# Kernel optimization log

Measured on AMD Instinct MI355X. Metric: run time of the kernel, lower is better.

## Reference

```python
import jax, jax.numpy as jnp
import numpy as np

B = 16384          # batch
S = 510            # no_of_states
D = 2 * S + 4      # 1024, context width
HID = 512          # self.hidden_size
H = 1024           # no_of_heads
INHIB = 3.0        # kWTA inhibition coefficient


def _lin(x, W, b):
    # torch nn.Linear convention: W is [out, in]
    return x @ W.T + b


def kwta(x, kw):
    """Per-row dynamic-k winner-take-all.
    k_i = argmax(kw[i]); top-k entries of x[i] kept, the rest divided by INHIB.
    Vectorized replacement for the original per-row topk + scatter loop."""
    k = jnp.argmax(kw, axis=1)                         # [B] per-row k
    s = -jnp.sort(-x, axis=1)                          # descending sort per row
    idx = jnp.clip(k - 1, 0, x.shape[1] - 1)
    thr = jnp.take_along_axis(s, idx[:, None], axis=1)  # k-th largest value
    mask = (x >= thr) & (k[:, None] > 0)               # winners (k=0 -> none)
    return jnp.where(mask, x, x / INHIB)


def setup_inputs() -> dict:
    key = jax.random.key(0)
    ks = jax.random.split(key, 30)

    def n(k, shape, s=0.02):
        return (jax.random.normal(k, shape) * s).astype(jnp.float32)

    return {
        "input": jax.random.normal(ks[0], (B, S), jnp.float32),
        "task_indicator": jax.random.normal(ks[1], (B, S + 4), jnp.float32),
        "hidden": jax.random.normal(ks[2], (1, B, D), jnp.float32),
        # Elman RNN step (single layer, hidden width D)
        "w_ih": n(ks[3], (D, D)), "b_ih": n(ks[4], (D,)),
        "w_hh": n(ks[5], (D, D)), "b_hh": n(ks[6], (D,)),
        # context gating heads
        "w_cx11": n(ks[7], (2 * HID, D)), "b_cx11": n(ks[8], (2 * HID,)),
        "w_cx12": n(ks[9], (2 * HID, 2 * HID)), "b_cx12": n(ks[10], (2 * HID,)),
        "w_cx21": n(ks[11], (HID, D)), "b_cx21": n(ks[12], (HID,)),
        "w_cx22": n(ks[13], (HID, HID)), "b_cx22": n(ks[14], (HID,)),
        "w_cx31": n(ks[15], (H, D)), "b_cx31": n(ks[16], (H,)),
        "w_cx32": n(ks[17], (H, H)), "b_cx32": n(ks[18], (H,)),
        # main MLP stack
        "w_l1": n(ks[19], (2 * HID, D)), "b_l1": n(ks[20], (2 * HID,)),
        "w_l2": n(ks[21], (HID, 2 * HID)), "b_l2": n(ks[22], (HID,)),
        "w_l3": n(ks[23], (H, HID)), "b_l3": n(ks[24], (H,)),
        "w_l4": n(ks[25], (H, H)), "b_l4": n(ks[26], (H,)),
    }


def reference(input, task_indicator, hidden,
              w_ih, b_ih, w_hh, b_hh,
              w_cx11, b_cx11, w_cx12, b_cx12,
              w_cx21, b_cx21, w_cx22, b_cx22,
              w_cx31, b_cx31, w_cx32, b_cx32,
              w_l1, b_l1, w_l2, b_l2, w_l3, b_l3, w_l4, b_l4):
    ctx = jnp.concatenate([input, task_indicator], axis=1)      # [B, D]
    h0 = hidden[0]                                              # [B, D]
    # Elman RNN step: out == next hidden state
    out = jnp.tanh(ctx @ w_ih.T + b_ih + h0 @ w_hh.T + b_hh)    # [B, D]
    next_hidden = out[:, None, :]                               # transpose(0,1) of [1,B,D]

    cx1 = jax.nn.softmax(_lin(jnp.tanh(_lin(out, w_cx11, b_cx11)), w_cx12, b_cx12), axis=1)
    cx2 = jax.nn.softmax(_lin(jnp.tanh(_lin(out, w_cx21, b_cx21)), w_cx22, b_cx22), axis=1)
    cx3 = jax.nn.softmax(_lin(jnp.tanh(_lin(out, w_cx31, b_cx31)), w_cx32, b_cx32), axis=1)

    x = _lin(out, w_l1, b_l1)        # [B, 2*HID]
    x = kwta(x, cx1)
    x = _lin(x, w_l2, b_l2)          # [B, HID]
    x = kwta(x, cx2)
    x = _lin(x, w_l3, b_l3)          # [B, H]
    x = kwta(x, cx3)
    x = _lin(x, w_l4, b_l4)          # [B, H]
    return (x, next_hidden)
```

## Files before the change

kernel.cpp:

```cpp
#include <hip/hip_runtime.h>
#include <math.h>

#define BB 16384
#define BM 128
#define BN 128
#define BK 32

__global__ __launch_bounds__(256) void concat_kernel(const float* __restrict__ inp,
    const float* __restrict__ task, float* __restrict__ ctx)
{
  int idx = blockIdx.x * 256 + threadIdx.x;
  int b = idx >> 10;
  int c = idx & 1023;
  float v;
  if (c < 510) v = inp[(size_t)b * 510 + c];
  else         v = task[(size_t)b * 514 + (c - 510)];
  ctx[idx] = v;
}

template<bool TANH, bool CIN>
__global__ __launch_bounds__(256) void gemm32g_kernel(
    const float* __restrict__ A, const float* __restrict__ W,
    const float* __restrict__ b1, const float* __restrict__ b2,
    const float* __restrict__ Cin, float* __restrict__ C,
    int N, int K, int lda, int ldw, unsigned foldmask)
{
  __shared__ float As[BK * BM];
  __shared__ float Bs[BK * BN];
  const int tid = threadIdx.x;
  const int tx = tid & 15;
  const int ty = tid >> 4;
  const int m0 = blockIdx.x * BM;
  const int n0 = blockIdx.y * BN;
  const int rrow = tid >> 3;
  const int kc = (tid & 7) << 2;

  float res[2][2][4][4], cur[2][2][4][4];
#pragma unroll
  for (int g = 0; g < 2; ++g)
#pragma unroll
    for (int h = 0; h < 2; ++h)
#pragma unroll
      for (int i = 0; i < 4; ++i)
#pragma unroll
        for (int j = 0; j < 4; ++j) { res[g][h][i][j] = 0.f; cur[g][h][i][j] = 0.f; }

  float4 ra[4], rb[4];
  const int NT = K / BK;

#pragma unroll
  for (int i = 0; i < 4; ++i) {
    int r = rrow + (i << 5);
    ra[i] = *(const float4*)(A + (size_t)(m0 + r) * lda + kc);
    rb[i] = *(const float4*)(W + (size_t)(n0 + r) * ldw + kc);
  }

  for (int kt = 0; kt < NT; ++kt) {
    __syncthreads();
#pragma unroll
    for (int i = 0; i < 4; ++i) {
      int cS = (rrow + (i << 5)) ^ kc;
      As[(kc + 0) * BM + cS] = ra[i].x;
      As[(kc + 1) * BM + cS] = ra[i].y;
      As[(kc + 2) * BM + cS] = ra[i].z;
      As[(kc + 3) * BM + cS] = ra[i].w;
      Bs[(kc + 0) * BN + cS] = rb[i].x;
      Bs[(kc + 1) * BN + cS] = rb[i].y;
      Bs[(kc + 2) * BN + cS] = rb[i].z;
      Bs[(kc + 3) * BN + cS] = rb[i].w;
    }
    __syncthreads();
    if (kt + 1 < NT) {
      int kb = (kt + 1) * BK;
#pragma unroll
      for (int i = 0; i < 4; ++i) {
        int r = rrow + (i << 5);
        ra[i] = *(const float4*)(A + (size_t)(m0 + r) * lda + kb + kc);
        rb[i] = *(const float4*)(W + (size_t)(n0 + r) * ldw + kb + kc);
      }
    }
#pragma unroll 8
    for (int kk = 0; kk < BK; ++kk) {
      const int swz = kk & 28;
      const float4 a0 = *(const float4*)&As[kk * BM + ((4 * ty) ^ swz)];
      const float4 a1 = *(const float4*)&As[kk * BM + 64 + ((4 * ty) ^ swz)];
      const float4 b0 = *(const float4*)&Bs[kk * BN + ((4 * tx) ^ swz)];
      const float4 b1r = *(const float4*)&Bs[kk * BN + 64 + ((4 * tx) ^ swz)];
      const float av[2][4] = {{a0.x, a0.y, a0.z, a0.w}, {a1.x, a1.y, a1.z, a1.w}};
      const float wv[2][4] = {{b0.x, b0.y, b0.z, b0.w}, {b1r.x, b1r.y, b1r.z, b1r.w}};
#pragma unroll
      for (int g = 0; g < 2; ++g)
#pragma unroll
        for (int h = 0; h < 2; ++h)
#pragma unroll
          for (int i = 0; i < 4; ++i)
#pragma unroll
            for (int j = 0; j < 4; ++j)
              cur[g][h][i][j] = fmaf(av[g][i], wv[h][j], cur[g][h][i][j]);
    }
    if ((foldmask >> kt) & 1u) {
#pragma unroll
      for (int g = 0; g < 2; ++g)
#pragma unroll
        for (int h = 0; h < 2; ++h)
#pragma unroll
          for (int i = 0; i < 4; ++i)
#pragma unroll
            for (int j = 0; j < 4; ++j) {
              res[g][h][i][j] = res[g][h][i][j] + cur[g][h][i][j];
              cur[g][h][i][j] = 0.f;
            }
    }
  }

  float4 b1v[2], b2v[2];
#pragma unroll
  for (int h = 0; h < 2; ++h) {
    int cb = n0 + h * 64 + 4 * tx;
    b1v[h] = b1 ? *(const float4*)&b1[cb] : make_float4(0.f, 0.f, 0.f, 0.f);
    b2v[h] = (CIN && b2) ? *(const float4*)&b2[cb] : make_float4(0.f, 0.f, 0.f, 0.f);
  }
#pragma unroll
  for (int g = 0; g < 2; ++g)
#pragma unroll
    for (int i = 0; i < 4; ++i) {
      int row = m0 + g * 64 + 4 * ty + i;
#pragma unroll
      for (int h = 0; h < 2; ++h) {
        int col = n0 + h * 64 + 4 * tx;
        float4 o;
        if (CIN) {
          float4 ci = *(const float4*)&Cin[(size_t)row * N + col];
          o.x = ((ci.x + b1v[h].x) + res[g][h][i][0]) + b2v[h].x;
          o.y = ((ci.y + b1v[h].y) + res[g][h][i][1]) + b2v[h].y;
          o.z = ((ci.z + b1v[h].z) + res[g][h][i][2]) + b2v[h].z;
          o.w = ((ci.w + b1v[h].w) + res[g][h][i][3]) + b2v[h].w;
        } else if (b1) {
          o.x = res[g][h][i][0] + b1v[h].x;
          o.y = res[g][h][i][1] + b1v[h].y;
          o.z = res[g][h][i][2] + b1v[h].z;
          o.w = res[g][h][i][3] + b1v[h].w;
        } else {
          o.x = res[g][h][i][0]; o.y = res[g][h][i][1];
          o.z = res[g][h][i][2]; o.w = res[g][h][i][3];
        }
        if (TANH) {
          o.x = (float)tanh((double)o.x);
          o.y = (float)tanh((double)o.y);
          o.z = (float)tanh((double)o.z);
          o.w = (float)tanh((double)o.w);
        }
        *(float4*)&C[(size_t)row * N + col] = o;
      }
    }
}

template<int NELEM>
__global__ __launch_bounds__(256) void kwta_kernel(const float* __restrict__ x,
    const float* __restrict__ cxz, float* __restrict__ out)
{
  constexpr int NPER = NELEM / 256;
  const int row = blockIdx.x;
  const int tid = threadIdx.x;
  const float* xr = x + (size_t)row * NELEM;
  const float* zr = cxz + (size_t)row * NELEM;
  float* orow = out + (size_t)row * NELEM;

  __shared__ float es[NELEM];
  __shared__ float red[256];
  __shared__ int   ri[256];
  __shared__ float bs[8];
  __shared__ float ssum;
  __shared__ unsigned hist[256];
  __shared__ unsigned cum[256];
  __shared__ int selBin;
  __shared__ unsigned selBase;

  float zv[NPER];
  float mx = -INFINITY;
#pragma unroll
  for (int j = 0; j < NPER; ++j) {
    zv[j] = zr[tid + (j << 8)];
    mx = fmaxf(mx, zv[j]);
  }
  red[tid] = mx;
  __syncthreads();
  for (int s = 128; s > 0; s >>= 1) {
    if (tid < s) red[tid] = fmaxf(red[tid], red[tid + s]);
    __syncthreads();
  }
  mx = red[0];
  __syncthreads();

  float ev[NPER];
#pragma unroll
  for (int j = 0; j < NPER; ++j) {
    float d = zv[j] - mx;
    ev[j] = (float)exp((double)d);
    es[tid + (j << 8)] = ev[j];
  }
  __syncthreads();

  if (tid < NELEM / 128) {
    const float* a = &es[tid * 128];
    float r0 = a[0], r1 = a[1], r2 = a[2], r3 = a[3];
    float r4 = a[4], r5 = a[5], r6 = a[6], r7 = a[7];
    for (int i = 8; i < 128; i += 8) {
      r0 += a[i + 0]; r1 += a[i + 1]; r2 += a[i + 2]; r3 += a[i + 3];
      r4 += a[i + 4]; r5 += a[i + 5]; r6 += a[i + 6]; r7 += a[i + 7];
    }
    bs[tid] = ((r0 + r1) + (r2 + r3)) + ((r4 + r5) + (r6 + r7));
  }
  __syncthreads();
  if (tid == 0) {
    float s;
    if (NELEM == 1024)
      s = ((bs[0] + bs[1]) + (bs[2] + bs[3])) + ((bs[4] + bs[5]) + (bs[6] + bs[7]));
    else
      s = (bs[0] + bs[1]) + (bs[2] + bs[3]);
    ssum = s;
  }
  __syncthreads();
  const float s = ssum;

  float bv = -INFINITY; int bi = 0x7fffffff;
#pragma unroll
  for (int j = 0; j < NPER; ++j) {
    float u = ev[j] / s;
    int i = tid + (j << 8);
    if (u > bv) { bv = u; bi = i; }
  }
  red[tid] = bv; ri[tid] = bi;
  __syncthreads();
  for (int st = 128; st > 0; st >>= 1) {
    if (tid < st) {
      float ov = red[tid + st]; int oi = ri[tid + st];
      if (ov > red[tid] || (ov == red[tid] && oi < ri[tid])) { red[tid] = ov; ri[tid] = oi; }
    }
    __syncthreads();
  }
  const int k = ri[0];

  float xv[NPER]; unsigned key[NPER];
#pragma unroll
  for (int j = 0; j < NPER; ++j) {
    float v = xr[tid + (j << 8)];
    xv[j] = v;
    unsigned sb = __float_as_uint(v);
    key[j] = (sb & 0x80000000u) ? ~sb : (sb | 0x80000000u);
  }

  float thr = 0.f;
  const bool kzero = (k == 0);
  if (!kzero) {
    unsigned ur = (unsigned)(NELEM - k);
    unsigned prefix = 0, pmask = 0;
    for (int shift = 24; shift >= 0; shift -= 8) {
      hist[tid] = 0;
      __syncthreads();
#pragma unroll
      for (int j = 0; j < NPER; ++j)
        if ((key[j] & pmask) == prefix) atomicAdd(&hist[(key[j] >> shift) & 255u], 1u);
      __syncthreads();
      unsigned v = hist[tid];
      cum[tid] = v;
      __syncthreads();
      for (int d = 1; d < 256; d <<= 1) {
        unsigned t = (tid >= d) ? cum[tid - d] : 0u;
        __syncthreads();
        v += t; cum[tid] = v;
        __syncthreads();
      }
      unsigned excl = v - hist[tid];
      if (ur >= excl && ur < v) { selBin = tid; selBase = excl; }
      __syncthreads();
      prefix |= ((unsigned)selBin) << shift;
      pmask  |= (255u << shift);
      ur -= selBase;
      __syncthreads();
    }
    thr = (prefix & 0x80000000u) ? __uint_as_float(prefix & 0x7FFFFFFFu)
                                 : __uint_as_float(~prefix);
  }
#pragma unroll
  for (int j = 0; j < NPER; ++j) {
    float v = xv[j];
    bool keep = !kzero && (v >= thr);
    orow[tid + (j << 8)] = keep ? v : (v / 3.0f);
  }
}

extern "C" void kernel_launch(void* const* d_in, const int* in_sizes, int n_in,
                              void* d_out, int out_size, void* d_ws, size_t ws_size,
                              hipStream_t stream) {
  const float* input  = (const float*)d_in[0];
  const float* task   = (const float*)d_in[1];
  const float* hidden = (const float*)d_in[2];
  const float* w_ih   = (const float*)d_in[3];  const float* b_ih   = (const float*)d_in[4];
  const float* w_hh   = (const float*)d_in[5];  const float* b_hh   = (const float*)d_in[6];
  const float* w_cx11 = (const float*)d_in[7];  const float* b_cx11 = (const float*)d_in[8];
  const float* w_cx12 = (const float*)d_in[9];  const float* b_cx12 = (const float*)d_in[10];
  const float* w_cx21 = (const float*)d_in[11]; const float* b_cx21 = (const float*)d_in[12];
  const float* w_cx22 = (const float*)d_in[13]; const float* b_cx22 = (const float*)d_in[14];
  const float* w_cx31 = (const float*)d_in[15]; const float* b_cx31 = (const float*)d_in[16];
  const float* w_cx32 = (const float*)d_in[17]; const float* b_cx32 = (const float*)d_in[18];
  const float* w_l1   = (const float*)d_in[19]; const float* b_l1   = (const float*)d_in[20];
  const float* w_l2   = (const float*)d_in[21]; const float* b_l2   = (const float*)d_in[22];
  const float* w_l3   = (const float*)d_in[23]; const float* b_l3   = (const float*)d_in[24];
  const float* w_l4   = (const float*)d_in[25]; const float* b_l4   = (const float*)d_in[26];

  float* out_x = (float*)d_out;
  float* out_h = out_x + (size_t)BB * 1024;

  int R = BB;
  while ((size_t)R * 8192 > ws_size && R > 128) R >>= 1;
  const int nChunks = BB / R;

  const unsigned FM1024 = (1u << 11) | (1u << 23) | (1u << 31);
  const unsigned FM512  = (1u << 11) | (1u << 15);

  dim3 blk(256);

  concat_kernel<<<BB * 1024 / 256, blk, 0, stream>>>(input, task, out_x);

  for (int c = 0; c < nChunks; ++c) {
    const size_t r0 = (size_t)c * R;
    float* S0 = (float*)d_ws;
    float* S1 = S0 + (size_t)R * 1024;
    float* S1hi = S1 + (size_t)R * 512;
    float* OX = out_x + r0 * 1024;
    const float* ctx_c = OX;
    const float* hid_c = hidden + r0 * 1024;
    float* out_c = out_h + r0 * 1024;
    dim3 g1024(R / BM, 1024 / BN);
    dim3 g512 (R / BM,  512 / BN);

    gemm32g_kernel<false, false><<<g1024, blk, 0, stream>>>(
        ctx_c, w_ih, nullptr, nullptr, nullptr, S0, 1024, 1024, 1024, 1024, FM1024);
    gemm32g_kernel<true, true><<<g1024, blk, 0, stream>>>(
        hid_c, w_hh, b_ih, b_hh, S0, out_c, 1024, 1024, 1024, 1024, FM1024);
    gemm32g_kernel<true, false><<<g1024, blk, 0, stream>>>(
        out_c, w_cx11, b_cx11, nullptr, nullptr, S1, 1024, 1024, 1024, 1024, FM1024);
    gemm32g_kernel<false, false><<<g1024, blk, 0, stream>>>(
        S1, w_cx12, b_cx12, nullptr, nullptr, S0, 1024, 1024, 1024, 1024, FM1024);
    gemm32g_kernel<false, false><<<g1024, blk, 0, stream>>>(
        out_c, w_l1, b_l1, nullptr, nullptr, OX, 1024, 1024, 1024, 1024, FM1024);
    kwta_kernel<1024><<<R, blk, 0, stream>>>(OX, S0, OX);
    gemm32g_kernel<true, false><<<g512, blk, 0, stream>>>(
        out_c, w_cx21, b_cx21, nullptr, nullptr, S1, 512, 1024, 1024, 1024, FM1024);
    gemm32g_kernel<false, false><<<g512, blk, 0, stream>>>(
        S1, w_cx22, b_cx22, nullptr, nullptr, S1hi, 512, 512, 512, 512, FM512);
    gemm32g_kernel<false, false><<<g512, blk, 0, stream>>>(
        OX, w_l2, b_l2, nullptr, nullptr, S0, 512, 1024, 1024, 1024, FM1024);
    kwta_kernel<512><<<R, blk, 0, stream>>>(S0, S1hi, S0);
    gemm32g_kernel<true, false><<<g1024, blk, 0, stream>>>(
        out_c, w_cx31, b_cx31, nullptr, nullptr, S1, 1024, 1024, 1024, 1024, FM1024);
    gemm32g_kernel<false, false><<<g1024, blk, 0, stream>>>(
        S1, w_cx32, b_cx32, nullptr, nullptr, OX, 1024, 1024, 1024, 1024, FM1024);
    gemm32g_kernel<false, false><<<g1024, blk, 0, stream>>>(
        S0, w_l3, b_l3, nullptr, nullptr, S1, 1024, 512, 512, 512, FM512);
    kwta_kernel<1024><<<R, blk, 0, stream>>>(S1, OX, S1);
    gemm32g_kernel<false, false><<<g1024, blk, 0, stream>>>(
        S1, w_l4, b_l4, nullptr, nullptr, OX, 1024, 1024, 1024, 1024, FM1024);
  }
}
```

Measured before the change: 4.555 ms.

## Halve GEMM M-tile to 64 and add XCD-aware workgroup swizzle

Shrinks the FP32 GEMM block tile from 128x128 to 64x128, so each thread holds a 4x8 accumulator set instead of 8x8 and there are twice as many workgroups. The flat workgroup index is remapped so that consecutive groups of blocks land on the same XCD, and the grid is transposed so the N dimension is the fast index. This aims to cut register pressure and raise occupancy while improving L2 reuse of weight and activation tiles. The cost is lower arithmetic intensity per LDS load (A/B reads per FMA rise) and more redundant global loads of the W tile.

```diff
diff --git a/kernel.cpp b/kernel.cpp
--- a/kernel.cpp
+++ b/kernel.cpp
@@ -2,7 +2,7 @@
 #include <math.h>
 
 #define BB 16384
-#define BM 128
+#define BM 64
 #define BN 128
 #define BK 32
 
@@ -30,40 +30,47 @@
   const int tid = threadIdx.x;
   const int tx = tid & 15;
   const int ty = tid >> 4;
-  const int m0 = blockIdx.x * BM;
-  const int n0 = blockIdx.y * BN;
+  const int gx = gridDim.x;
+  const int nwg = gx * gridDim.y;
+  const int flat = blockIdx.y * gx + blockIdx.x;
+  const int cpx = nwg >> 3;
+  const int swb = (flat & 7) * cpx + (flat >> 3);
+  const int m0 = (swb / gx) * BM;
+  const int n0 = (swb % gx) * BN;
   const int rrow = tid >> 3;
   const int kc = (tid & 7) << 2;
 
-  float res[2][2][4][4], cur[2][2][4][4];
-#pragma unroll
-  for (int g = 0; g < 2; ++g)
-#pragma unroll
-    for (int h = 0; h < 2; ++h)
-#pragma unroll
-      for (int i = 0; i < 4; ++i)
-#pragma unroll
-        for (int j = 0; j < 4; ++j) { res[g][h][i][j] = 0.f; cur[g][h][i][j] = 0.f; }
-
-  float4 ra[4], rb[4];
+  float res[2][4][4], cur[2][4][4];
+#pragma unroll
+  for (int h = 0; h < 2; ++h)
+#pragma unroll
+    for (int i = 0; i < 4; ++i)
+#pragma unroll
+      for (int j = 0; j < 4; ++j) { res[h][i][j] = 0.f; cur[h][i][j] = 0.f; }
+
+  float4 ra[2], rb[4];
   const int NT = K / BK;
 
 #pragma unroll
-  for (int i = 0; i < 4; ++i) {
-    int r = rrow + (i << 5);
-    ra[i] = *(const float4*)(A + (size_t)(m0 + r) * lda + kc);
-    rb[i] = *(const float4*)(W + (size_t)(n0 + r) * ldw + kc);
-  }
+  for (int i = 0; i < 2; ++i)
+    ra[i] = *(const float4*)(A + (size_t)(m0 + rrow + (i << 5)) * lda + kc);
+#pragma unroll
+  for (int i = 0; i < 4; ++i)
+    rb[i] = *(const float4*)(W + (size_t)(n0 + rrow + (i << 5)) * ldw + kc);
 
   for (int kt = 0; kt < NT; ++kt) {
     __syncthreads();
 #pragma unroll
-    for (int i = 0; i < 4; ++i) {
+    for (int i = 0; i < 2; ++i) {
       int cS = (rrow + (i << 5)) ^ kc;
       As[(kc + 0) * BM + cS] = ra[i].x;
       As[(kc + 1) * BM + cS] = ra[i].y;
       As[(kc + 2) * BM + cS] = ra[i].z;
       As[(kc + 3) * BM + cS] = ra[i].w;
+    }
+#pragma unroll
+    for (int i = 0; i < 4; ++i) {
+      int cS = (rrow + (i << 5)) ^ kc;
       Bs[(kc + 0) * BN + cS] = rb[i].x;
       Bs[(kc + 1) * BN + cS] = rb[i].y;
       Bs[(kc + 2) * BN + cS] = rb[i].z;
@@ -73,43 +80,38 @@
     if (kt + 1 < NT) {
       int kb = (kt + 1) * BK;
 #pragma unroll
-      for (int i = 0; i < 4; ++i) {
-        int r = rrow + (i << 5);
-        ra[i] = *(const float4*)(A + (size_t)(m0 + r) * lda + kb + kc);
-        rb[i] = *(const float4*)(W + (size_t)(n0 + r) * ldw + kb + kc);
-      }
+      for (int i = 0; i < 2; ++i)
+        ra[i] = *(const float4*)(A + (size_t)(m0 + rrow + (i << 5)) * lda + kb + kc);
+#pragma unroll
+      for (int i = 0; i < 4; ++i)
+        rb[i] = *(const float4*)(W + (size_t)(n0 + rrow + (i << 5)) * ldw + kb + kc);
     }
 #pragma unroll 8
     for (int kk = 0; kk < BK; ++kk) {
       const int swz = kk & 28;
       const float4 a0 = *(const float4*)&As[kk * BM + ((4 * ty) ^ swz)];
-      const float4 a1 = *(const float4*)&As[kk * BM + 64 + ((4 * ty) ^ swz)];
       const float4 b0 = *(const float4*)&Bs[kk * BN + ((4 * tx) ^ swz)];
       const float4 b1r = *(const float4*)&Bs[kk * BN + 64 + ((4 * tx) ^ swz)];
-      const float av[2][4] = {{a0.x, a0.y, a0.z, a0.w}, {a1.x, a1.y, a1.z, a1.w}};
+      const float av[4] = {a0.x, a0.y, a0.z, a0.w};
       const float wv[2][4] = {{b0.x, b0.y, b0.z, b0.w}, {b1r.x, b1r.y, b1r.z, b1r.w}};
 #pragma unroll
-      for (int g = 0; g < 2; ++g)
-#pragma unroll
-        for (int h = 0; h < 2; ++h)
-#pragma unroll
-          for (int i = 0; i < 4; ++i)
-#pragma unroll
-            for (int j = 0; j < 4; ++j)
-              cur[g][h][i][j] = fmaf(av[g][i], wv[h][j], cur[g][h][i][j]);
+      for (int h = 0; h < 2; ++h)
+#pragma unroll
+        for (int i = 0; i < 4; ++i)
+#pragma unroll
+          for (int j = 0; j < 4; ++j)
+            cur[h][i][j] = fmaf(av[i], wv[h][j], cur[h][i][j]);
     }
     if ((foldmask >> kt) & 1u) {
 #pragma unroll
-      for (int g = 0; g < 2; ++g)
-#pragma unroll
-        for (int h = 0; h < 2; ++h)
-#pragma unroll
-          for (int i = 0; i < 4; ++i)
-#pragma unroll
-            for (int j = 0; j < 4; ++j) {
-              res[g][h][i][j] = res[g][h][i][j] + cur[g][h][i][j];
-              cur[g][h][i][j] = 0.f;
-            }
+      for (int h = 0; h < 2; ++h)
+#pragma unroll
+        for (int i = 0; i < 4; ++i)
+#pragma unroll
+          for (int j = 0; j < 4; ++j) {
+            res[h][i][j] = res[h][i][j] + cur[h][i][j];
+            cur[h][i][j] = 0.f;
+          }
     }
   }
 
@@ -121,38 +123,36 @@
     b2v[h] = (CIN && b2) ? *(const float4*)&b2[cb] : make_float4(0.f, 0.f, 0.f, 0.f);
   }
 #pragma unroll
-  for (int g = 0; g < 2; ++g)
-#pragma unroll
-    for (int i = 0; i < 4; ++i) {
-      int row = m0 + g * 64 + 4 * ty + i;
-#pragma unroll
-      for (int h = 0; h < 2; ++h) {
-        int col = n0 + h * 64 + 4 * tx;
-        float4 o;
-        if (CIN) {
-          float4 ci = *(const float4*)&Cin[(size_t)row * N + col];
-          o.x = ((ci.x + b1v[h].x) + res[g][h][i][0]) + b2v[h].x;
-          o.y = ((ci.y + b1v[h].y) + res[g][h][i][1]) + b2v[h].y;
-          o.z = ((ci.z + b1v[h].z) + res[g][h][i][2]) + b2v[h].z;
-          o.w = ((ci.w + b1v[h].w) + res[g][h][i][3]) + b2v[h].w;
-        } else if (b1) {
-          o.x = res[g][h][i][0] + b1v[h].x;
-          o.y = res[g][h][i][1] + b1v[h].y;
-          o.z = res[g][h][i][2] + b1v[h].z;
-          o.w = res[g][h][i][3] + b1v[h].w;
-        } else {
-          o.x = res[g][h][i][0]; o.y = res[g][h][i][1];
-          o.z = res[g][h][i][2]; o.w = res[g][h][i][3];
-        }
-        if (TANH) {
-          o.x = (float)tanh((double)o.x);
-          o.y = (float)tanh((double)o.y);
-          o.z = (float)tanh((double)o.z);
-          o.w = (float)tanh((double)o.w);
-        }
-        *(float4*)&C[(size_t)row * N + col] = o;
+  for (int i = 0; i < 4; ++i) {
+    int row = m0 + 4 * ty + i;
+#pragma unroll
+    for (int h = 0; h < 2; ++h) {
+      int col = n0 + h * 64 + 4 * tx;
+      float4 o;
+      if (CIN) {
+        float4 ci = *(const float4*)&Cin[(size_t)row * N + col];
+        o.x = ((ci.x + b1v[h].x) + res[h][i][0]) + b2v[h].x;
+        o.y = ((ci.y + b1v[h].y) + res[h][i][1]) + b2v[h].y;
+        o.z = ((ci.z + b1v[h].z) + res[h][i][2]) + b2v[h].z;
+        o.w = ((ci.w + b1v[h].w) + res[h][i][3]) + b2v[h].w;
+      } else if (b1) {
+        o.x = res[h][i][0] + b1v[h].x;
+        o.y = res[h][i][1] + b1v[h].y;
+        o.z = res[h][i][2] + b1v[h].z;
+        o.w = res[h][i][3] + b1v[h].w;
+      } else {
+        o.x = res[h][i][0]; o.y = res[h][i][1];
+        o.z = res[h][i][2]; o.w = res[h][i][3];
       }
-    }
+      if (TANH) {
+        o.x = (float)tanh((double)o.x);
+        o.y = (float)tanh((double)o.y);
+        o.z = (float)tanh((double)o.z);
+        o.w = (float)tanh((double)o.w);
+      }
+      *(float4*)&C[(size_t)row * N + col] = o;
+    }
+  }
 }
 
 template<int NELEM>
@@ -332,8 +332,8 @@
     const float* ctx_c = OX;
     const float* hid_c = hidden + r0 * 1024;
     float* out_c = out_h + r0 * 1024;
-    dim3 g1024(R / BM, 1024 / BN);
-    dim3 g512 (R / BM,  512 / BN);
+    dim3 g1024(1024 / BN, R / BM);
+    dim3 g512 ( 512 / BN, R / BM);
 
     gemm32g_kernel<false, false><<<g1024, blk, 0, stream>>>(
         ctx_c, w_ih, nullptr, nullptr, nullptr, S0, 1024, 1024, 1024, 1024, FM1024);
```

Result: slower. 4.819 ms (+5.8%).

## Use packed FP32 FMA in GEMM inner loop and XCD-aware block swizzle

Applied to the files above, without the earlier changes.

Rewrites the GEMM accumulators as 2-wide float vectors and uses elementwise vector FMA, so the compiler can emit packed FP32 FMA instructions (v_pk_fma_f32) and issue half as many FMA instructions. It also remaps workgroup IDs so consecutive blocks land on the same XCD, and swaps grid dimensions so N tiles vary fastest, aiming for better L2 reuse of A rows. The packed form may constrain register allocation, and the swizzle assumes the block count is divisible by 8.

```diff
diff --git a/kernel.cpp b/kernel.cpp
--- a/kernel.cpp
+++ b/kernel.cpp
@@ -5,6 +5,8 @@
 #define BM 128
 #define BN 128
 #define BK 32
+
+typedef float f32x2 __attribute__((ext_vector_type(2)));
 
 __global__ __launch_bounds__(256) void concat_kernel(const float* __restrict__ inp,
     const float* __restrict__ task, float* __restrict__ ctx)
@@ -30,12 +32,17 @@
   const int tid = threadIdx.x;
   const int tx = tid & 15;
   const int ty = tid >> 4;
-  const int m0 = blockIdx.x * BM;
-  const int n0 = blockIdx.y * BN;
+  const int gx = gridDim.x;
+  const int nwg = gx * gridDim.y;
+  const int flat = blockIdx.y * gx + blockIdx.x;
+  const int cpx = nwg >> 3;
+  const int swb = (flat & 7) * cpx + (flat >> 3);
+  const int m0 = (swb / gx) * BM;
+  const int n0 = (swb % gx) * BN;
   const int rrow = tid >> 3;
   const int kc = (tid & 7) << 2;
 
-  float res[2][2][4][4], cur[2][2][4][4];
+  f32x2 res[2][2][4][2], cur[2][2][4][2];
 #pragma unroll
   for (int g = 0; g < 2; ++g)
 #pragma unroll
@@ -43,7 +50,10 @@
 #pragma unroll
       for (int i = 0; i < 4; ++i)
 #pragma unroll
-        for (int j = 0; j < 4; ++j) { res[g][h][i][j] = 0.f; cur[g][h][i][j] = 0.f; }
+        for (int jp = 0; jp < 2; ++jp) {
+          res[g][h][i][jp] = (f32x2){0.f, 0.f};
+          cur[g][h][i][jp] = (f32x2){0.f, 0.f};
+        }
 
   float4 ra[4], rb[4];
   const int NT = K / BK;
@@ -87,28 +97,32 @@
       const float4 b0 = *(const float4*)&Bs[kk * BN + ((4 * tx) ^ swz)];
       const float4 b1r = *(const float4*)&Bs[kk * BN + 64 + ((4 * tx) ^ swz)];
       const float av[2][4] = {{a0.x, a0.y, a0.z, a0.w}, {a1.x, a1.y, a1.z, a1.w}};
-      const float wv[2][4] = {{b0.x, b0.y, b0.z, b0.w}, {b1r.x, b1r.y, b1r.z, b1r.w}};
+      const f32x2 wv2[2][2] = {{(f32x2){b0.x, b0.y}, (f32x2){b0.z, b0.w}},
+                               {(f32x2){b1r.x, b1r.y}, (f32x2){b1r.z, b1r.w}}};
 #pragma unroll
       for (int g = 0; g < 2; ++g)
 #pragma unroll
+        for (int i = 0; i < 4; ++i) {
+          const f32x2 as = (f32x2){av[g][i], av[g][i]};
+#pragma unroll
+          for (int h = 0; h < 2; ++h)
+#pragma unroll
+            for (int jp = 0; jp < 2; ++jp)
+              cur[g][h][i][jp] =
+                  __builtin_elementwise_fma(as, wv2[h][jp], cur[g][h][i][jp]);
+        }
+    }
+    if ((foldmask >> kt) & 1u) {
+#pragma unroll
+      for (int g = 0; g < 2; ++g)
+#pragma unroll
         for (int h = 0; h < 2; ++h)
 #pragma unroll
           for (int i = 0; i < 4; ++i)
 #pragma unroll
-            for (int j = 0; j < 4; ++j)
-              cur[g][h][i][j] = fmaf(av[g][i], wv[h][j], cur[g][h][i][j]);
-    }
-    if ((foldmask >> kt) & 1u) {
-#pragma unroll
-      for (int g = 0; g < 2; ++g)
-#pragma unroll
-        for (int h = 0; h < 2; ++h)
-#pragma unroll
-          for (int i = 0; i < 4; ++i)
-#pragma unroll
-            for (int j = 0; j < 4; ++j) {
-              res[g][h][i][j] = res[g][h][i][j] + cur[g][h][i][j];
-              cur[g][h][i][j] = 0.f;
+            for (int jp = 0; jp < 2; ++jp) {
+              res[g][h][i][jp] = res[g][h][i][jp] + cur[g][h][i][jp];
+              cur[g][h][i][jp] = (f32x2){0.f, 0.f};
             }
     }
   }
@@ -128,21 +142,22 @@
 #pragma unroll
       for (int h = 0; h < 2; ++h) {
         int col = n0 + h * 64 + 4 * tx;
+        const float rs[4] = {res[g][h][i][0][0], res[g][h][i][0][1],
+                             res[g][h][i][1][0], res[g][h][i][1][1]};
         float4 o;
         if (CIN) {
           float4 ci = *(const float4*)&Cin[(size_t)row * N + col];
-          o.x = ((ci.x + b1v[h].x) + res[g][h][i][0]) + b2v[h].x;
-          o.y = ((ci.y + b1v[h].y) + res[g][h][i][1]) + b2v[h].y;
-          o.z = ((ci.z + b1v[h].z) + res[g][h][i][2]) + b2v[h].z;
-          o.w = ((ci.w + b1v[h].w) + res[g][h][i][3]) + b2v[h].w;
+          o.x = ((ci.x + b1v[h].x) + rs[0]) + b2v[h].x;
+          o.y = ((ci.y + b1v[h].y) + rs[1]) + b2v[h].y;
+          o.z = ((ci.z + b1v[h].z) + rs[2]) + b2v[h].z;
+          o.w = ((ci.w + b1v[h].w) + rs[3]) + b2v[h].w;
         } else if (b1) {
-          o.x = res[g][h][i][0] + b1v[h].x;
-          o.y = res[g][h][i][1] + b1v[h].y;
-          o.z = res[g][h][i][2] + b1v[h].z;
-          o.w = res[g][h][i][3] + b1v[h].w;
+          o.x = rs[0] + b1v[h].x;
+          o.y = rs[1] + b1v[h].y;
+          o.z = rs[2] + b1v[h].z;
+          o.w = rs[3] + b1v[h].w;
         } else {
-          o.x = res[g][h][i][0]; o.y = res[g][h][i][1];
-          o.z = res[g][h][i][2]; o.w = res[g][h][i][3];
+          o.x = rs[0]; o.y = rs[1]; o.z = rs[2]; o.w = rs[3];
         }
         if (TANH) {
           o.x = (float)tanh((double)o.x);
@@ -332,8 +347,8 @@
     const float* ctx_c = OX;
     const float* hid_c = hidden + r0 * 1024;
     float* out_c = out_h + r0 * 1024;
-    dim3 g1024(R / BM, 1024 / BN);
-    dim3 g512 (R / BM,  512 / BN);
+    dim3 g1024(1024 / BN, R / BM);
+    dim3 g512 ( 512 / BN, R / BM);
 
     gemm32g_kernel<false, false><<<g1024, blk, 0, stream>>>(
         ctx_c, w_ih, nullptr, nullptr, nullptr, S0, 1024, 1024, 1024, 1024, FM1024);
```

Result: no change. 4.528 ms (-0.6%).
